# Performance work log

Measured on AMD Instinct MI355X. Metric: run time of the kernel, lower is better.

Reference implementation:

```python
import jax, jax.numpy as jnp
import numpy as np

N = 100000   # nodes
E = 800000   # edges
D_IN = 128   # input feature dim
H = 128      # GCN hidden units
M = 256      # MLP hidden
L = 40       # num_labels


def setup_inputs() -> dict:
    key = jax.random.key(0)
    ks = jax.random.split(key, 16)
    inp = {
        "x": jax.random.normal(ks[0], (N, D_IN), dtype=jnp.float32),
        "edge_index": jax.random.randint(ks[1], (2, E), 0, N, dtype=jnp.int32),
        "edge_weight": jax.random.uniform(ks[2], (E,), dtype=jnp.float32),
    }
    def glorot(k, shape):
        lim = np.sqrt(6.0 / (shape[0] + shape[1])).astype(np.float32)
        return jax.random.uniform(k, shape, jnp.float32, -lim, lim)
    inp["W0"] = glorot(ks[3], (D_IN, H)); inp["b0"] = jnp.zeros((H,), jnp.float32)
    inp["W1"] = glorot(ks[4], (H, H));    inp["b1"] = jnp.zeros((H,), jnp.float32)
    inp["W2"] = glorot(ks[5], (H, H));    inp["b2"] = jnp.zeros((H,), jnp.float32)
    inp["Wm0"] = glorot(ks[6], (H, M));   inp["bm0"] = jnp.zeros((M,), jnp.float32)
    inp["Wm1"] = glorot(ks[7], (M, L));   inp["bm1"] = jnp.zeros((L,), jnp.float32)
    return inp


def _gcn_norm(edge_index, edge_weight):
    # renorm trick: add self-loops (weight 1.0), then sym-normalize
    loop = jnp.arange(N, dtype=edge_index.dtype)
    row = jnp.concatenate([edge_index[0], loop])
    col = jnp.concatenate([edge_index[1], loop])
    w = jnp.concatenate([edge_weight, jnp.ones((N,), edge_weight.dtype)])
    deg = jax.ops.segment_sum(w, row, num_segments=N)
    dinv = jnp.where(deg > 0, jax.lax.rsqrt(deg), 0.0)
    norm = dinv[row] * w * dinv[col]
    return row, col, norm


def _gcn_layer(h, row, col, norm, W, b):
    h = h @ W                                   # [N, H]
    msg = h[col] * norm[:, None]                # gather + scale, [E+N, H]
    agg = jax.ops.segment_sum(msg, row, num_segments=N)
    return jax.nn.relu(agg + b)


def reference(x, edge_index, edge_weight, W0, b0, W1, b1, W2, b2, Wm0, bm0, Wm1, bm1):
    row, col, norm = _gcn_norm(edge_index, edge_weight)
    h = _gcn_layer(x, row, col, norm, W0, b0)
    h = _gcn_layer(h, row, col, norm, W1, b1)
    h = _gcn_layer(h, row, col, norm, W2, b2)
    h = jax.nn.relu(h @ Wm0 + bm0)              # MLP hidden
    return h @ Wm1 + bm1                        # logits [N, L]
```

## Files before the change

### kernel.cpp

```cpp
#include <hip/hip_runtime.h>
#include <hip/hip_fp16.h>
#include <math.h>

#define CAP 32
typedef unsigned short ushort_t;
typedef __attribute__((ext_vector_type(8))) short bf16x8;
typedef __attribute__((ext_vector_type(4))) float f32x4;

__device__ inline float bf2f_lo(unsigned u) { return __uint_as_float(u << 16); }
__device__ inline float bf2f_hi(unsigned u) { return __uint_as_float(u & 0xffff0000u); }
__device__ inline unsigned bf16rne(float f) {
    unsigned u = __float_as_uint(f);
    return (u + 0x7fffu + ((u >> 16) & 1u)) >> 16;
}
__device__ inline float dec_w(unsigned p) {
    return __half2float(__ushort_as_half((ushort_t)(p & 0x7fffu)));
}
__device__ inline bf16x8 u4_to_bf(uint4 u) {
    union { uint4 u; bf16x8 b; } cv; cv.u = u; return cv.b;
}
__device__ inline void accum8(float acc[8], uint4 u, float nm) {
    acc[0] = fmaf(bf2f_lo(u.x), nm, acc[0]);
    acc[1] = fmaf(bf2f_hi(u.x), nm, acc[1]);
    acc[2] = fmaf(bf2f_lo(u.y), nm, acc[2]);
    acc[3] = fmaf(bf2f_hi(u.y), nm, acc[3]);
    acc[4] = fmaf(bf2f_lo(u.z), nm, acc[4]);
    acc[5] = fmaf(bf2f_hi(u.z), nm, acc[5]);
    acc[6] = fmaf(bf2f_lo(u.w), nm, acc[6]);
    acc[7] = fmaf(bf2f_hi(u.w), nm, acc[7]);
}

__global__ __launch_bounds__(256) void k_setup(
    const float* __restrict__ W0, const float* __restrict__ W1,
    const float* __restrict__ W2, const float* __restrict__ Wm0,
    const float* __restrict__ Wm1,
    ushort_t* __restrict__ W0t, ushort_t* __restrict__ W1t,
    ushort_t* __restrict__ W2t, ushort_t* __restrict__ Wm0t,
    ushort_t* __restrict__ Wm1t)
{
    const int S0 = 128 * 128, S1 = 256 * 128, S2 = 256 * 40;
    int total = 3 * S0 + S1 + S2;
    for (int idx = blockIdx.x * 256 + threadIdx.x; idx < total; idx += gridDim.x * 256) {
        int i = idx;
        const float* W; ushort_t* Wt; int K, N;
        if (i < S0)            { W = W0;  Wt = W0t;  K = 128; N = 128; }
        else if (i < 2 * S0)   { W = W1;  Wt = W1t;  K = 128; N = 128; i -= S0; }
        else if (i < 3 * S0)   { W = W2;  Wt = W2t;  K = 128; N = 128; i -= 2 * S0; }
        else if (i < 3 * S0 + S1) { W = Wm0; Wt = Wm0t; K = 128; N = 256; i -= 3 * S0; }
        else                   { W = Wm1; Wt = Wm1t; K = 256; N = 40;  i -= 3 * S0 + S1; }
        int k = i / N, c = i - k * N;
        Wt[(size_t)c * K + k] = (ushort_t)bf16rne(W[(size_t)k * N + c]);
    }
}

__global__ __launch_bounds__(256) void k_prep2(const unsigned* __restrict__ bucket,
    const int* __restrict__ cursor, float* __restrict__ dinv, int n)
{
    int gid = blockIdx.x * 256 + threadIdx.x;
    int node = gid >> 4;
    if (node >= n) return;
    int f = gid & 15;
    int c = cursor[node]; if (c > CAP) c = CAP;
    float d = 0.f;
    int j0 = 2 * f;
    uint2 p = *(const uint2*)(bucket + (size_t)node * CAP + j0);
    if (j0 < c)     d += dec_w(p.x);
    if (j0 + 1 < c) d += dec_w(p.y);
    #pragma unroll
    for (int m = 1; m < 16; m <<= 1) d += __shfl_xor(d, m, 16);
    if (f == 0) dinv[node] = 1.0f / sqrtf(1.0f + d);
}

__global__ __launch_bounds__(256) void k_norm2(unsigned* __restrict__ bucket,
    const int* __restrict__ cnt, const float* __restrict__ dinv, int n)
{
    int gid = blockIdx.x * 256 + threadIdx.x;
    int node = gid >> 4, lj = gid & 15;
    if (node >= n) return;
    int c = cnt[node]; if (c > CAP) c = CAP;
    #pragma unroll
    for (int j = lj; j < c; j += 16) {
        unsigned p = bucket[(size_t)node * CAP + j];
        float wn = dec_w(p) * dinv[p >> 15];
        bucket[(size_t)node * CAP + j] =
            (p & 0xffff8000u) | (unsigned)__half_as_ushort(__float2half(wn));
    }
}

__global__ __launch_bounds__(256, 4) void k_fill_gemm1(
    const int* __restrict__ erow, const int* __restrict__ ecol,
    const float* __restrict__ ew, int* __restrict__ cursor,
    unsigned* __restrict__ bucket, int e,
    const float* __restrict__ x, const ushort_t* __restrict__ Wt,
    ushort_t* __restrict__ Cb, int n, int nbg, int K)
{
    __shared__ ushort_t Wsb[128 * 128];
    const int tid = threadIdx.x;
    const int bid = blockIdx.x;
    if (bid % K != 0) {
        int fb = bid - bid / K - 1;
        int i = fb * 256 + tid;
        if (i < e) {
            int r = erow[i];
            int pos = atomicAdd(&cursor[r], 1);
            if (pos < CAP) {
                unsigned hb = (unsigned)__half_as_ushort(__float2half(ew[i]));
                bucket[(size_t)r * CAP + pos] = ((unsigned)ecol[i] << 15) | hb;
            }
        }
        return;
    }
    const int gb = bid / K;
    if (gb >= nbg) return;
    const int row0 = gb * 128;
    {
        const int rl = tid >> 4, ch = tid & 15;
        #pragma unroll
        for (int it = 0; it < 8; ++it) {
            int c = it * 16 + rl;
            uint4 u = *(const uint4*)(Wt + (size_t)c * 128 + ch * 8);
            *(uint4*)&Wsb[(c * 128 + ch * 8) ^ ((c & 7) << 3)] = u;
        }
    }
    __syncthreads();

    const int lane = tid & 63;
    const int wv = tid >> 6;
    const int lm = lane & 15;
    const int lk = (lane >> 4) * 8;
    int g0 = row0 + wv * 32 + lm;
    int g1 = g0 + 16;
    size_t x0 = (size_t)((g0 < n) ? g0 : 0) * 128;
    size_t x1 = (size_t)((g1 < n) ? g1 : 0) * 128;

    f32x4 acc[2][8];
    #pragma unroll
    for (int m = 0; m < 2; ++m)
        #pragma unroll
        for (int t = 0; t < 8; ++t) acc[m][t] = (f32x4){0.f, 0.f, 0.f, 0.f};

    #pragma unroll
    for (int kk = 0; kk < 4; ++kk) {
        int k0 = kk * 32 + lk;
        const float4* s0 = (const float4*)(x + x0 + k0);
        const float4* s1 = (const float4*)(x + x1 + k0);
        float4 v0 = s0[0], v1 = s0[1], v2 = s1[0], v3 = s1[1];
        uint4 p0, p1;
        p0.x = bf16rne(v0.x) | (bf16rne(v0.y) << 16);
        p0.y = bf16rne(v0.z) | (bf16rne(v0.w) << 16);
        p0.z = bf16rne(v1.x) | (bf16rne(v1.y) << 16);
        p0.w = bf16rne(v1.z) | (bf16rne(v1.w) << 16);
        p1.x = bf16rne(v2.x) | (bf16rne(v2.y) << 16);
        p1.y = bf16rne(v2.z) | (bf16rne(v2.w) << 16);
        p1.z = bf16rne(v3.x) | (bf16rne(v3.y) << 16);
        p1.w = bf16rne(v3.z) | (bf16rne(v3.w) << 16);
        bf16x8 a0 = u4_to_bf(p0), a1 = u4_to_bf(p1);
        #pragma unroll
        for (int t = 0; t < 8; ++t) {
            int c = t * 16 + lm;
            bf16x8 b = *(const bf16x8*)&Wsb[(c * 128 + k0) ^ ((c & 7) << 3)];
            acc[0][t] = __builtin_amdgcn_mfma_f32_16x16x32_bf16(a0, b, acc[0][t], 0, 0, 0);
            acc[1][t] = __builtin_amdgcn_mfma_f32_16x16x32_bf16(a1, b, acc[1][t], 0, 0, 0);
        }
    }
    #pragma unroll
    for (int m = 0; m < 2; ++m) {
        #pragma unroll
        for (int j = 0; j < 4; ++j) {
            int gr = row0 + wv * 32 + m * 16 + (lane >> 4) * 4 + j;
            if (gr < n) {
                #pragma unroll
                for (int t = 0; t < 8; ++t)
                    Cb[(size_t)gr * 128 + t * 16 + lm] = (ushort_t)bf16rne(acc[m][t][j]);
            }
        }
    }
}

__global__ __launch_bounds__(256) void k_agg(const ushort_t* __restrict__ hWb,
    const int* __restrict__ cnt, const unsigned* __restrict__ bucket,
    const float* __restrict__ dinv, const float* __restrict__ preb,
    ushort_t* __restrict__ outb, int n)
{
    int gid = blockIdx.x * 256 + threadIdx.x;
    int node = gid >> 4;
    if (node >= n) return;
    int f8 = gid & 15;
    int c = cnt[node]; if (c > CAP) c = CAP;
    size_t s = (size_t)node * CAP, t = s + c;
    float dn = dinv[node];
    float acc[8];
    #pragma unroll
    for (int i = 0; i < 8; ++i) acc[i] = 0.f;
    {
        uint4 v = *(const uint4*)(hWb + (size_t)node * 128 + f8 * 8);
        accum8(acc, v, dn);
    }
    size_t j = s;
    for (; j + 3 < t; j += 4) {
        uint4 q = *(const uint4*)(bucket + j);
        uint4 u0 = *(const uint4*)(hWb + (size_t)(q.x >> 15) * 128 + f8 * 8);
        uint4 u1 = *(const uint4*)(hWb + (size_t)(q.y >> 15) * 128 + f8 * 8);
        uint4 u2 = *(const uint4*)(hWb + (size_t)(q.z >> 15) * 128 + f8 * 8);
        uint4 u3 = *(const uint4*)(hWb + (size_t)(q.w >> 15) * 128 + f8 * 8);
        accum8(acc, u0, dec_w(q.x));
        accum8(acc, u1, dec_w(q.y));
        accum8(acc, u2, dec_w(q.z));
        accum8(acc, u3, dec_w(q.w));
    }
    for (; j < t; ++j) {
        unsigned p = bucket[j];
        uint4 u = *(const uint4*)(hWb + (size_t)(p >> 15) * 128 + f8 * 8);
        accum8(acc, u, dec_w(p));
    }
    float4 b0 = *(const float4*)(preb + f8 * 8);
    float4 b1 = *(const float4*)(preb + f8 * 8 + 4);
    uint4 pk;
    pk.x = bf16rne(fmaxf(fmaf(acc[0], dn, b0.x), 0.f))
         | (bf16rne(fmaxf(fmaf(acc[1], dn, b0.y), 0.f)) << 16);
    pk.y = bf16rne(fmaxf(fmaf(acc[2], dn, b0.z), 0.f))
         | (bf16rne(fmaxf(fmaf(acc[3], dn, b0.w), 0.f)) << 16);
    pk.z = bf16rne(fmaxf(fmaf(acc[4], dn, b1.x), 0.f))
         | (bf16rne(fmaxf(fmaf(acc[5], dn, b1.y), 0.f)) << 16);
    pk.w = bf16rne(fmaxf(fmaf(acc[6], dn, b1.z), 0.f))
         | (bf16rne(fmaxf(fmaf(acc[7], dn, b1.w), 0.f)) << 16);
    *(uint4*)(outb + (size_t)node * 128 + f8 * 8) = pk;
}

__global__ __launch_bounds__(256, 4) void k_gemm_bb(
    const ushort_t* __restrict__ Ab, const ushort_t* __restrict__ Wt,
    const float* __restrict__ postb, int postrelu,
    ushort_t* __restrict__ Cb, int cstride, int n)
{
    __shared__ ushort_t Wsb[128 * 128];
    const int row0 = blockIdx.x * 128;
    const int wcol0 = blockIdx.y * 128;
    const float* pbp = postb ? postb + wcol0 : (const float*)0;
    const int tid = threadIdx.x;
    {
        const int rl = tid >> 4, ch = tid & 15;
        #pragma unroll
        for (int it = 0; it < 8; ++it) {
            int c = it * 16 + rl;
            uint4 u = *(const uint4*)(Wt + (size_t)(wcol0 + c) * 128 + ch * 8);
            *(uint4*)&Wsb[(c * 128 + ch * 8) ^ ((c & 7) << 3)] = u;
        }
    }
    __syncthreads();

    const int lane = tid & 63;
    const int wv = tid >> 6;
    const int lm = lane & 15;
    const int lk = (lane >> 4) * 8;
    int g0 = row0 + wv * 32 + lm;
    int g1 = g0 + 16;
    size_t a0base = (size_t)((g0 < n) ? g0 : 0) * 128;
    size_t a1base = (size_t)((g1 < n) ? g1 : 0) * 128;

    f32x4 acc[2][8];
    #pragma unroll
    for (int m = 0; m < 2; ++m)
        #pragma unroll
        for (int t = 0; t < 8; ++t) acc[m][t] = (f32x4){0.f, 0.f, 0.f, 0.f};

    #pragma unroll
    for (int kk = 0; kk < 4; ++kk) {
        int k0 = kk * 32 + lk;
        bf16x8 a0 = *(const bf16x8*)(Ab + a0base + k0);
        bf16x8 a1 = *(const bf16x8*)(Ab + a1base + k0);
        #pragma unroll
        for (int t = 0; t < 8; ++t) {
            int c = t * 16 + lm;
            bf16x8 b = *(const bf16x8*)&Wsb[(c * 128 + k0) ^ ((c & 7) << 3)];
            acc[0][t] = __builtin_amdgcn_mfma_f32_16x16x32_bf16(a0, b, acc[0][t], 0, 0, 0);
            acc[1][t] = __builtin_amdgcn_mfma_f32_16x16x32_bf16(a1, b, acc[1][t], 0, 0, 0);
        }
    }

    float pb[8];
    #pragma unroll
    for (int t = 0; t < 8; ++t) pb[t] = pbp ? pbp[t * 16 + lm] : 0.f;

    #pragma unroll
    for (int m = 0; m < 2; ++m) {
        #pragma unroll
        for (int j = 0; j < 4; ++j) {
            int gr = row0 + wv * 32 + m * 16 + (lane >> 4) * 4 + j;
            if (gr < n) {
                #pragma unroll
                for (int t = 0; t < 8; ++t) {
                    float o = acc[m][t][j] + pb[t];
                    if (postrelu) o = fmaxf(o, 0.f);
                    Cb[(size_t)gr * cstride + wcol0 + t * 16 + lm] = (ushort_t)bf16rne(o);
                }
            }
        }
    }
}

__global__ __launch_bounds__(256) void k_final_mfma(
    const ushort_t* __restrict__ hidb, const ushort_t* __restrict__ Wt,
    const float* __restrict__ bias, float* __restrict__ C, int n)
{
    __shared__ ushort_t Asb[128 * 64];
    const int row0 = blockIdx.x * 128;
    const int tid = threadIdx.x;
    const int lane = tid & 63;
    const int wv = tid >> 6;
    const int lm = lane & 15;
    const int lk8 = (lane >> 4) * 8;

    bf16x8 wfrag[3][8];
    #pragma unroll
    for (int t = 0; t < 3; ++t) {
        int col = t * 16 + lm;
        #pragma unroll
        for (int ks = 0; ks < 8; ++ks) {
            if (col < 40)
                wfrag[t][ks] = *(const bf16x8*)(Wt + (size_t)col * 256 + ks * 32 + lk8);
            else
                wfrag[t][ks] = (bf16x8){0, 0, 0, 0, 0, 0, 0, 0};
        }
    }

    f32x4 acc[2][3];
    #pragma unroll
    for (int m = 0; m < 2; ++m)
        #pragma unroll
        for (int t = 0; t < 3; ++t) acc[m][t] = (f32x4){0.f, 0.f, 0.f, 0.f};

    for (int kb = 0; kb < 256; kb += 64) {
        __syncthreads();
        for (int it = 0; it < 4; ++it) {
            int i = tid + it * 256;
            int r = i >> 3, ch = i & 7;
            int gr = row0 + r;
            uint4 u = make_uint4(0, 0, 0, 0);
            if (gr < n) u = *(const uint4*)(hidb + (size_t)gr * 256 + kb + ch * 8);
            *(uint4*)&Asb[(r * 64 + ch * 8) ^ ((r & 7) << 3)] = u;
        }
        __syncthreads();
        #pragma unroll
        for (int ks = 0; ks < 2; ++ks) {
            int k0 = ks * 32 + lk8;
            int ksg = (kb >> 5) + ks;
            #pragma unroll
            for (int m = 0; m < 2; ++m) {
                int r = (wv * 2 + m) * 16 + lm;
                bf16x8 a = *(const bf16x8*)&Asb[(r * 64 + k0) ^ ((r & 7) << 3)];
                #pragma unroll
                for (int t = 0; t < 3; ++t)
                    acc[m][t] = __builtin_amdgcn_mfma_f32_16x16x32_bf16(
                        a, wfrag[t][ksg], acc[m][t], 0, 0, 0);
            }
        }
    }

    #pragma unroll
    for (int m = 0; m < 2; ++m) {
        int grb = row0 + (wv * 2 + m) * 16 + (lane >> 4) * 4;
        #pragma unroll
        for (int t = 0; t < 3; ++t) {
            int col = t * 16 + lm;
            if (col < 40) {
                float pb = bias[col];
                #pragma unroll
                for (int j = 0; j < 4; ++j) {
                    int gr = grb + j;
                    if (gr < n) C[(size_t)gr * 40 + col] = acc[m][t][j] + pb;
                }
            }
        }
    }
}


extern "C" void kernel_launch(void* const* d_in, const int* in_sizes, int n_in,
                              void* d_out, int out_size, void* d_ws, size_t ws_size,
                              hipStream_t stream)
{
    const float* x   = (const float*)d_in[0];
    const int*   ei  = (const int*)d_in[1];
    const float* ew  = (const float*)d_in[2];
    const float* W0  = (const float*)d_in[3];
    const float* b0  = (const float*)d_in[4];
    const float* W1  = (const float*)d_in[5];
    const float* b1  = (const float*)d_in[6];
    const float* W2  = (const float*)d_in[7];
    const float* b2  = (const float*)d_in[8];
    const float* Wm0 = (const float*)d_in[9];
    const float* bm0 = (const float*)d_in[10];
    const float* Wm1 = (const float*)d_in[11];
    const float* bm1 = (const float*)d_in[12];
    float* out = (float*)d_out;

    const int n = in_sizes[0] / 128;
    const int e = in_sizes[2];
    const int* erow = ei;
    const int* ecol = ei + e;

    char* ws = (char*)d_ws;
    size_t actB = (size_t)n * 128 * sizeof(ushort_t);
    size_t hidB = (size_t)n * 256 * sizeof(ushort_t);
    size_t bktB = (size_t)n * CAP * 4;
    size_t wtElems = (size_t)3 * 128 * 128 + 256 * 128 + 40 * 256;
    size_t need = 2 * actB + hidB + bktB + (size_t)2 * n * 4 + wtElems * 2;
    if (ws_size < need) return;

    ushort_t* B1     = (ushort_t*)ws;
    ushort_t* B2     = (ushort_t*)(ws + actB);
    ushort_t* hidb   = (ushort_t*)(ws + 2 * actB);
    unsigned* bucket = (unsigned*)(ws + 2 * actB + hidB);
    float*    dinv   = (float*)(ws + 2 * actB + hidB + bktB);
    int*      cursor = (int*)(dinv + n);
    ushort_t* W0t    = (ushort_t*)(cursor + n);
    ushort_t* W1t    = W0t + 128 * 128;
    ushort_t* W2t    = W1t + 128 * 128;
    ushort_t* Wm0t   = W2t + 128 * 128;
    ushort_t* Wm1t   = Wm0t + 256 * 128;

    dim3 blk(256);
    int nb_e = (e + 255) / 256;
    int nb_pn = (n * 16 + 255) / 256;
    int nb_agg = (n * 16 + 255) / 256;
    int nb_g = (n + 127) / 128;

    hipMemsetAsync(cursor, 0, (size_t)n * 4, stream);
    k_setup<<<360, blk, 0, stream>>>(W0, W1, W2, Wm0, Wm1, W0t, W1t, W2t, Wm0t, Wm1t);

    int K = nb_e / nb_g + 2;
    int nb_fg = nb_g * K;
    k_fill_gemm1<<<nb_fg, blk, 0, stream>>>(erow, ecol, ew, cursor, bucket, e,
                                            x, W0t, B1, n, nb_g, K);
    k_prep2<<<nb_pn, blk, 0, stream>>>(bucket, cursor, dinv, n);
    k_norm2<<<nb_pn, blk, 0, stream>>>(bucket, cursor, dinv, n);

    k_agg<<<nb_agg, blk, 0, stream>>>(B1, cursor, bucket, dinv, b0, B2, n);
    k_gemm_bb<<<dim3(nb_g, 1), blk, 0, stream>>>(B2, W1t, nullptr, 0, B1, 128, n);
    k_agg<<<nb_agg, blk, 0, stream>>>(B1, cursor, bucket, dinv, b1, B2, n);
    k_gemm_bb<<<dim3(nb_g, 1), blk, 0, stream>>>(B2, W2t, nullptr, 0, B1, 128, n);
    k_agg<<<nb_agg, blk, 0, stream>>>(B1, cursor, bucket, dinv, b2, B2, n);
    k_gemm_bb<<<dim3(nb_g, 2), blk, 0, stream>>>(B2, Wm0t, bm0, 1, hidb, 256, n);
    k_final_mfma<<<nb_g, blk, 0, stream>>>(hidb, Wm1t, bm1, out, n);
}
```

Measured before the change: 268.2 us.

## Fuse MLP layers into one kernel and fold column norm into aggregation

Replaces the two MLP kernels with one fused kernel. It computes the 256-wide hidden layer into shared memory (64KB) and applies the final 40-wide projection from there, so the N×256 hidden tensor never round-trips through global memory. It also removes the separate k_norm2 pass by multiplying each edge weight by dinv[col] inside the aggregation loops. The cost is an extra dinv gather per edge in each of three aggregation passes, plus higher shared-memory and register use in the fused kernel, which may lower occupancy.

```diff
diff --git a/kernel.cpp b/kernel.cpp
--- a/kernel.cpp
+++ b/kernel.cpp
@@ -69,22 +69,6 @@
     #pragma unroll
     for (int m = 1; m < 16; m <<= 1) d += __shfl_xor(d, m, 16);
     if (f == 0) dinv[node] = 1.0f / sqrtf(1.0f + d);
-}
-
-__global__ __launch_bounds__(256) void k_norm2(unsigned* __restrict__ bucket,
-    const int* __restrict__ cnt, const float* __restrict__ dinv, int n)
-{
-    int gid = blockIdx.x * 256 + threadIdx.x;
-    int node = gid >> 4, lj = gid & 15;
-    if (node >= n) return;
-    int c = cnt[node]; if (c > CAP) c = CAP;
-    #pragma unroll
-    for (int j = lj; j < c; j += 16) {
-        unsigned p = bucket[(size_t)node * CAP + j];
-        float wn = dec_w(p) * dinv[p >> 15];
-        bucket[(size_t)node * CAP + j] =
-            (p & 0xffff8000u) | (unsigned)__half_as_ushort(__float2half(wn));
-    }
 }
 
 __global__ __launch_bounds__(256, 4) void k_fill_gemm1(
@@ -203,15 +187,15 @@
         uint4 u1 = *(const uint4*)(hWb + (size_t)(q.y >> 15) * 128 + f8 * 8);
         uint4 u2 = *(const uint4*)(hWb + (size_t)(q.z >> 15) * 128 + f8 * 8);
         uint4 u3 = *(const uint4*)(hWb + (size_t)(q.w >> 15) * 128 + f8 * 8);
-        accum8(acc, u0, dec_w(q.x));
-        accum8(acc, u1, dec_w(q.y));
-        accum8(acc, u2, dec_w(q.z));
-        accum8(acc, u3, dec_w(q.w));
+        accum8(acc, u0, dec_w(q.x) * dinv[q.x >> 15]);
+        accum8(acc, u1, dec_w(q.y) * dinv[q.y >> 15]);
+        accum8(acc, u2, dec_w(q.z) * dinv[q.z >> 15]);
+        accum8(acc, u3, dec_w(q.w) * dinv[q.w >> 15]);
     }
     for (; j < t; ++j) {
         unsigned p = bucket[j];
         uint4 u = *(const uint4*)(hWb + (size_t)(p >> 15) * 128 + f8 * 8);
-        accum8(acc, u, dec_w(p));
+        accum8(acc, u, dec_w(p) * dinv[p >> 15]);
     }
     float4 b0 = *(const float4*)(preb + f8 * 8);
     float4 b1 = *(const float4*)(preb + f8 * 8 + 4);
@@ -229,20 +213,17 @@
 
 __global__ __launch_bounds__(256, 4) void k_gemm_bb(
     const ushort_t* __restrict__ Ab, const ushort_t* __restrict__ Wt,
-    const float* __restrict__ postb, int postrelu,
-    ushort_t* __restrict__ Cb, int cstride, int n)
+    ushort_t* __restrict__ Cb, int n)
 {
     __shared__ ushort_t Wsb[128 * 128];
     const int row0 = blockIdx.x * 128;
-    const int wcol0 = blockIdx.y * 128;
-    const float* pbp = postb ? postb + wcol0 : (const float*)0;
     const int tid = threadIdx.x;
     {
         const int rl = tid >> 4, ch = tid & 15;
         #pragma unroll
         for (int it = 0; it < 8; ++it) {
             int c = it * 16 + rl;
-            uint4 u = *(const uint4*)(Wt + (size_t)(wcol0 + c) * 128 + ch * 8);
+            uint4 u = *(const uint4*)(Wt + (size_t)c * 128 + ch * 8);
             *(uint4*)&Wsb[(c * 128 + ch * 8) ^ ((c & 7) << 3)] = u;
         }
     }
@@ -277,10 +258,6 @@
         }
     }
 
-    float pb[8];
-    #pragma unroll
-    for (int t = 0; t < 8; ++t) pb[t] = pbp ? pbp[t * 16 + lm] : 0.f;
-
     #pragma unroll
     for (int m = 0; m < 2; ++m) {
         #pragma unroll
@@ -288,27 +265,78 @@
             int gr = row0 + wv * 32 + m * 16 + (lane >> 4) * 4 + j;
             if (gr < n) {
                 #pragma unroll
-                for (int t = 0; t < 8; ++t) {
-                    float o = acc[m][t][j] + pb[t];
-                    if (postrelu) o = fmaxf(o, 0.f);
-                    Cb[(size_t)gr * cstride + wcol0 + t * 16 + lm] = (ushort_t)bf16rne(o);
-                }
+                for (int t = 0; t < 8; ++t)
+                    Cb[(size_t)gr * 128 + t * 16 + lm] = (ushort_t)bf16rne(acc[m][t][j]);
             }
         }
     }
 }
 
-__global__ __launch_bounds__(256) void k_final_mfma(
-    const ushort_t* __restrict__ hidb, const ushort_t* __restrict__ Wt,
-    const float* __restrict__ bias, float* __restrict__ C, int n)
-{
-    __shared__ ushort_t Asb[128 * 64];
+__global__ __launch_bounds__(256) void k_mlp_final(
+    const ushort_t* __restrict__ Ab, const ushort_t* __restrict__ Wm0t,
+    const float* __restrict__ bm0,
+    const ushort_t* __restrict__ Wm1t,
+    const float* __restrict__ bm1, float* __restrict__ out, int n)
+{
+    __shared__ ushort_t sbuf[256 * 128];
     const int row0 = blockIdx.x * 128;
     const int tid = threadIdx.x;
     const int lane = tid & 63;
     const int wv = tid >> 6;
     const int lm = lane & 15;
-    const int lk8 = (lane >> 4) * 8;
+    const int lk = (lane >> 4) * 8;
+
+    {
+        const int rl = tid >> 4, ch = tid & 15;
+        #pragma unroll
+        for (int it = 0; it < 16; ++it) {
+            int c = it * 16 + rl;
+            uint4 u = *(const uint4*)(Wm0t + (size_t)c * 128 + ch * 8);
+            *(uint4*)&sbuf[(c * 128 + ch * 8) ^ ((c & 7) << 3)] = u;
+        }
+    }
+    __syncthreads();
+
+    int g0 = row0 + wv * 32 + lm;
+    int g1 = g0 + 16;
+    size_t a0base = (size_t)((g0 < n) ? g0 : 0) * 128;
+    size_t a1base = (size_t)((g1 < n) ? g1 : 0) * 128;
+
+    f32x4 acc[2][16];
+    #pragma unroll
+    for (int m = 0; m < 2; ++m)
+        #pragma unroll
+        for (int t = 0; t < 16; ++t) acc[m][t] = (f32x4){0.f, 0.f, 0.f, 0.f};
+
+    #pragma unroll
+    for (int kk = 0; kk < 4; ++kk) {
+        int k0 = kk * 32 + lk;
+        bf16x8 a0 = *(const bf16x8*)(Ab + a0base + k0);
+        bf16x8 a1 = *(const bf16x8*)(Ab + a1base + k0);
+        #pragma unroll
+        for (int t = 0; t < 16; ++t) {
+            int c = t * 16 + lm;
+            bf16x8 b = *(const bf16x8*)&sbuf[(c * 128 + k0) ^ ((c & 7) << 3)];
+            acc[0][t] = __builtin_amdgcn_mfma_f32_16x16x32_bf16(a0, b, acc[0][t], 0, 0, 0);
+            acc[1][t] = __builtin_amdgcn_mfma_f32_16x16x32_bf16(a1, b, acc[1][t], 0, 0, 0);
+        }
+    }
+    __syncthreads();
+
+    #pragma unroll
+    for (int m = 0; m < 2; ++m) {
+        #pragma unroll
+        for (int j = 0; j < 4; ++j) {
+            int r = wv * 32 + m * 16 + (lane >> 4) * 4 + j;
+            #pragma unroll
+            for (int t = 0; t < 16; ++t) {
+                int col = t * 16 + lm;
+                float o = fmaxf(acc[m][t][j] + bm0[col], 0.f);
+                sbuf[(r * 256 + col) ^ ((r & 7) << 3)] = (ushort_t)bf16rne(o);
+            }
+        }
+    }
+    __syncthreads();
 
     bf16x8 wfrag[3][8];
     #pragma unroll
@@ -317,57 +345,43 @@
         #pragma unroll
         for (int ks = 0; ks < 8; ++ks) {
             if (col < 40)
-                wfrag[t][ks] = *(const bf16x8*)(Wt + (size_t)col * 256 + ks * 32 + lk8);
+                wfrag[t][ks] = *(const bf16x8*)(Wm1t + (size_t)col * 256 + ks * 32 + lk);
             else
                 wfrag[t][ks] = (bf16x8){0, 0, 0, 0, 0, 0, 0, 0};
         }
     }
 
-    f32x4 acc[2][3];
+    f32x4 acc2[2][3];
     #pragma unroll
     for (int m = 0; m < 2; ++m)
         #pragma unroll
-        for (int t = 0; t < 3; ++t) acc[m][t] = (f32x4){0.f, 0.f, 0.f, 0.f};
-
-    for (int kb = 0; kb < 256; kb += 64) {
-        __syncthreads();
-        for (int it = 0; it < 4; ++it) {
-            int i = tid + it * 256;
-            int r = i >> 3, ch = i & 7;
-            int gr = row0 + r;
-            uint4 u = make_uint4(0, 0, 0, 0);
-            if (gr < n) u = *(const uint4*)(hidb + (size_t)gr * 256 + kb + ch * 8);
-            *(uint4*)&Asb[(r * 64 + ch * 8) ^ ((r & 7) << 3)] = u;
-        }
-        __syncthreads();
-        #pragma unroll
-        for (int ks = 0; ks < 2; ++ks) {
-            int k0 = ks * 32 + lk8;
-            int ksg = (kb >> 5) + ks;
+        for (int t = 0; t < 3; ++t) acc2[m][t] = (f32x4){0.f, 0.f, 0.f, 0.f};
+
+    #pragma unroll
+    for (int ks = 0; ks < 8; ++ks) {
+        #pragma unroll
+        for (int m = 0; m < 2; ++m) {
+            int r = wv * 32 + m * 16 + lm;
+            bf16x8 a = *(const bf16x8*)&sbuf[(r * 256 + ks * 32 + lk) ^ ((r & 7) << 3)];
             #pragma unroll
-            for (int m = 0; m < 2; ++m) {
-                int r = (wv * 2 + m) * 16 + lm;
-                bf16x8 a = *(const bf16x8*)&Asb[(r * 64 + k0) ^ ((r & 7) << 3)];
-                #pragma unroll
-                for (int t = 0; t < 3; ++t)
-                    acc[m][t] = __builtin_amdgcn_mfma_f32_16x16x32_bf16(
-                        a, wfrag[t][ksg], acc[m][t], 0, 0, 0);
-            }
+            for (int t = 0; t < 3; ++t)
+                acc2[m][t] = __builtin_amdgcn_mfma_f32_16x16x32_bf16(
+                    a, wfrag[t][ks], acc2[m][t], 0, 0, 0);
         }
     }
 
     #pragma unroll
     for (int m = 0; m < 2; ++m) {
-        int grb = row0 + (wv * 2 + m) * 16 + (lane >> 4) * 4;
+        int grb = row0 + wv * 32 + m * 16 + (lane >> 4) * 4;
         #pragma unroll
         for (int t = 0; t < 3; ++t) {
             int col = t * 16 + lm;
             if (col < 40) {
-                float pb = bias[col];
+                float pb = bm1[col];
                 #pragma unroll
                 for (int j = 0; j < 4; ++j) {
                     int gr = grb + j;
-                    if (gr < n) C[(size_t)gr * 40 + col] = acc[m][t][j] + pb;
+                    if (gr < n) out[(size_t)gr * 40 + col] = acc2[m][t][j] + pb;
                 }
             }
         }
@@ -409,7 +423,6 @@
 
     ushort_t* B1     = (ushort_t*)ws;
     ushort_t* B2     = (ushort_t*)(ws + actB);
-    ushort_t* hidb   = (ushort_t*)(ws + 2 * actB);
     unsigned* bucket = (unsigned*)(ws + 2 * actB + hidB);
     float*    dinv   = (float*)(ws + 2 * actB + hidB + bktB);
     int*      cursor = (int*)(dinv + n);
@@ -433,13 +446,11 @@
     k_fill_gemm1<<<nb_fg, blk, 0, stream>>>(erow, ecol, ew, cursor, bucket, e,
                                             x, W0t, B1, n, nb_g, K);
     k_prep2<<<nb_pn, blk, 0, stream>>>(bucket, cursor, dinv, n);
-    k_norm2<<<nb_pn, blk, 0, stream>>>(bucket, cursor, dinv, n);
 
     k_agg<<<nb_agg, blk, 0, stream>>>(B1, cursor, bucket, dinv, b0, B2, n);
-    k_gemm_bb<<<dim3(nb_g, 1), blk, 0, stream>>>(B2, W1t, nullptr, 0, B1, 128, n);
+    k_gemm_bb<<<nb_g, blk, 0, stream>>>(B2, W1t, B1, n);
     k_agg<<<nb_agg, blk, 0, stream>>>(B1, cursor, bucket, dinv, b1, B2, n);
-    k_gemm_bb<<<dim3(nb_g, 1), blk, 0, stream>>>(B2, W2t, nullptr, 0, B1, 128, n);
+    k_gemm_bb<<<nb_g, blk, 0, stream>>>(B2, W2t, B1, n);
     k_agg<<<nb_agg, blk, 0, stream>>>(B1, cursor, bucket, dinv, b2, B2, n);
-    k_gemm_bb<<<dim3(nb_g, 2), blk, 0, stream>>>(B2, Wm0t, bm0, 1, hidb, 256, n);
-    k_final_mfma<<<nb_g, blk, 0, stream>>>(hidb, Wm1t, bm1, out, n);
-}
+    k_mlp_final<<<nb_g, blk, 0, stream>>>(B2, Wm0t, bm0, Wm1t, bm1, out, n);
+}
```

Measured after the change: 283.3 us. 1.06x slower.
